# Kernel optimization log

Hardware: AMD Instinct MI355X
Metric: run time of the kernel (lower is better)

Reference implementation:

```python
import jax, jax.numpy as jnp
import numpy as np

B, T = 32, 1024
AC, SE, H, NH = 20, 16, 64, 4
HD = H // NH  # 16


def setup_inputs() -> dict:
    key = jax.random.key(0)
    ks = jax.random.split(key, 8)
    g = 0.1  # xavier gain used in _init_weights (rough scale)
    return {
        'acoustic': jax.random.normal(ks[0], (B, T, AC), jnp.float32),
        'semantic': jax.random.normal(ks[1], (B, T, SE), jnp.float32),
        'Wq': jax.random.normal(ks[2], (H, SE), jnp.float32) * g,
        'bq': jnp.zeros((H,), jnp.float32),
        'Wkv': jax.random.normal(ks[3], (2 * H, AC), jnp.float32) * g,
        'bkv': jnp.zeros((2 * H,), jnp.float32),
        'in_w': jax.random.normal(ks[4], (3 * H, H), jnp.float32) * g,
        'in_b': jnp.zeros((3 * H,), jnp.float32),
        'out_w': jax.random.normal(ks[5], (H, H), jnp.float32) * g,
        'out_b': jnp.zeros((H,), jnp.float32),
        'proj_w': jax.random.normal(ks[6], (AC, H), jnp.float32) * g,
        'proj_b': jnp.zeros((AC,), jnp.float32),
        'residual_logit': jnp.float32(-2.0),
        'ln_gamma': jnp.ones((AC,), jnp.float32),
        'ln_beta': jnp.zeros((AC,), jnp.float32),
    }


def _std(x, axis, keepdims=True):
    # torch.std default: unbiased (ddof=1)
    return jnp.std(x, axis=axis, ddof=1, keepdims=keepdims)


def reference(acoustic, semantic, Wq, bq, Wkv, bkv, in_w, in_b, out_w, out_b,
              proj_w, proj_b, residual_logit, ln_gamma, ln_beta):
    # projections to hidden space
    q = semantic @ Wq.T + bq                       # [B,T,H]
    kv = acoustic @ Wkv.T + bkv                    # [B,T,2H]
    k, v = kv[..., :H], kv[..., H:]
    # nn.MultiheadAttention in-projection
    qi = q @ in_w[:H].T + in_b[:H]
    ki = k @ in_w[H:2 * H].T + in_b[H:2 * H]
    vi = v @ in_w[2 * H:].T + in_b[2 * H:]
    # split heads -> [B,T,NH,HD]
    qh = qi.reshape(B, T, NH, HD)
    kh = ki.reshape(B, T, NH, HD)
    vh = vi.reshape(B, T, NH, HD)
    scores = jnp.einsum('bqhd,bkhd->bhqk', qh, kh) / jnp.sqrt(jnp.float32(HD))
    attn = jax.nn.softmax(scores, axis=-1)         # [B,NH,T,T]
    ctx = jnp.einsum('bhqk,bkhd->bqhd', attn, vh).reshape(B, T, H)
    attended = ctx @ out_w.T + out_b               # MHA out_proj
    enhanced_raw = attended @ proj_w.T + proj_b    # [B,T,AC]
    enhanced = acoustic + jax.nn.sigmoid(residual_logit) * enhanced_raw

    # statistics over batch+time (no_grad in torch -> stop_gradient)
    orig_mean = jax.lax.stop_gradient(jnp.mean(acoustic, axis=(0, 1), keepdims=True))
    orig_std = jax.lax.stop_gradient(_std(acoustic, (0, 1)) + 1e-8)
    a_n = (acoustic - orig_mean) / orig_std
    e_n = (enhanced - orig_mean) / orig_std
    std_ratio = _std(e_n, (0, 1)) / (_std(a_n, (0, 1)) + 1e-8)
    std_corr = jnp.where(std_ratio < 0.4, 0.4 / std_ratio, jnp.ones_like(std_ratio))
    enhanced_final = (e_n * std_corr) * orig_std + orig_mean

    # LayerNorm over last dim (biased variance, eps=1e-5)
    mu = jnp.mean(enhanced_final, axis=-1, keepdims=True)
    var = jnp.mean(jnp.square(enhanced_final - mu), axis=-1, keepdims=True)
    return (enhanced_final - mu) * jax.lax.rsqrt(var + 1e-5) * ln_gamma + ln_beta
```

## Files before the change

### kernel.cpp

```cpp
#include <hip/hip_runtime.h>
#include <hip/hip_bf16.h>
#include <math.h>

#define B 32
#define T 1024
#define AC 20
#define SE 16
#define H 64
#define NH 4
#define HD 16
#define NROW (B*T)
#define BH (B*NH)
#define NCHUNK (T/32)
#define NSLOT 128

typedef unsigned short u16;
typedef short short8 __attribute__((ext_vector_type(8)));
typedef float f32x16 __attribute__((ext_vector_type(16)));
typedef unsigned int uintx4 __attribute__((ext_vector_type(4)));

#define F_QB   (BH*T*16/2)
#define OFF_QB   0
#define OFF_KB   (OFF_QB + F_QB)
#define OFF_VT   (OFF_KB + F_QB)
#define OFF_ET   (OFF_VT + F_QB)
#define OFF_WF   (OFF_ET + AC*NROW)
#define OFF_ACC  (OFF_WF + 5120)
#define OFF_ST   (OFF_ACC + NSLOT*80)

#define WF_WQ 0
#define WF_BQ 1024
#define WF_WK 1088
#define WF_BK 2368
#define WF_WV 2432
#define WF_BV 3712
#define WF_WO 3776
#define WF_BO 5056
#define WF_TOTAL 5076

__device__ __forceinline__ u16 bf16b(float a) {
    __hip_bfloat16 t = __float2bfloat16(a);
    u16 u; __builtin_memcpy(&u, &t, 2); return u;
}
__device__ __forceinline__ unsigned packbf(float a, float b) {
    return (unsigned)bf16b(a) | ((unsigned)bf16b(b) << 16);
}

__global__ __launch_bounds__(256) void k_fuse(
    const float* __restrict__ Wq, const float* __restrict__ bq,
    const float* __restrict__ Wkv, const float* __restrict__ bkv,
    const float* __restrict__ in_w, const float* __restrict__ in_b,
    const float* __restrict__ out_w, const float* __restrict__ out_b,
    const float* __restrict__ proj_w, const float* __restrict__ proj_b,
    float* __restrict__ wf, float* __restrict__ accum) {
    int idx = blockIdx.x * 256 + threadIdx.x;
    if (idx < NSLOT*40) {
        accum[idx] = 0.f;
        accum[idx + NSLOT*40] = 0.f;
    }
    if (idx >= WF_TOTAL) return;
    if (idx < WF_BQ) {
        int i = idx >> 4, j = idx & 15;
        float s = 0.f;
        for (int m = 0; m < H; ++m) s += in_w[i*H + m] * Wq[m*SE + j];
        wf[idx] = 0.25f * s;
    } else if (idx < WF_WK) {
        int i = idx - WF_BQ;
        float s = in_b[i];
        for (int m = 0; m < H; ++m) s += in_w[i*H + m] * bq[m];
        wf[idx] = 0.25f * s;
    } else if (idx < WF_BK) {
        int r = idx - WF_WK; int i = r / AC, j = r % AC;
        float s = 0.f;
        for (int m = 0; m < H; ++m) s += in_w[(H+i)*H + m] * Wkv[m*AC + j];
        wf[idx] = s;
    } else if (idx < WF_WV) {
        int i = idx - WF_BK;
        float s = in_b[H + i];
        for (int m = 0; m < H; ++m) s += in_w[(H+i)*H + m] * bkv[m];
        wf[idx] = s;
    } else if (idx < WF_BV) {
        int r = idx - WF_WV; int i = r / AC, j = r % AC;
        float s = 0.f;
        for (int m = 0; m < H; ++m) s += in_w[(2*H+i)*H + m] * Wkv[(H+m)*AC + j];
        wf[idx] = s;
    } else if (idx < WF_WO) {
        int i = idx - WF_BV;
        float s = in_b[2*H + i];
        for (int m = 0; m < H; ++m) s += in_w[(2*H+i)*H + m] * bkv[H + m];
        wf[idx] = s;
    } else if (idx < WF_BO) {
        int r = idx - WF_WO; int c = r >> 6, d = r & 63;
        float s = 0.f;
        for (int m = 0; m < H; ++m) s += proj_w[c*H + m] * out_w[m*H + d];
        wf[idx] = s;
    } else {
        int c = idx - WF_BO;
        float s = proj_b[c];
        for (int m = 0; m < H; ++m) s += proj_w[c*H + m] * out_b[m];
        wf[idx] = s;
    }
}

__global__ __launch_bounds__(192) void k_qkv(
    const float* __restrict__ sem, const float* __restrict__ acst,
    const float* __restrict__ wf,
    u16* __restrict__ Qb, u16* __restrict__ Kb, u16* __restrict__ Vtb) {
    const int tid = threadIdx.x;
    const int sec = tid >> 4, r = tid & 15;
    const int row = blockIdx.x * 16 + r;
    const int b = row >> 10, t = row & 1023;
    const int type = sec >> 2, h = sec & 3;
    float o[16];
    if (type == 0) {
        float s[SE];
        const float4* sp = (const float4*)(sem + (size_t)row * SE);
        #pragma unroll
        for (int i = 0; i < 4; ++i) {
            float4 v = sp[i];
            s[4*i] = v.x; s[4*i+1] = v.y; s[4*i+2] = v.z; s[4*i+3] = v.w;
        }
        const float* wq = wf + WF_WQ + h*16*SE;
        const float* bq = wf + WF_BQ + h*16;
        #pragma unroll
        for (int ii = 0; ii < 16; ++ii) {
            float acc = bq[ii];
            #pragma unroll
            for (int j = 0; j < 4; ++j) {
                float4 w4 = *(const float4*)(wq + ii*SE + 4*j);
                acc += s[4*j]*w4.x + s[4*j+1]*w4.y + s[4*j+2]*w4.z + s[4*j+3]*w4.w;
            }
            o[ii] = acc;
        }
        unsigned* dst = (unsigned*)(Qb + (((size_t)(b*NH + h))*T + t)*16);
        #pragma unroll
        for (int i = 0; i < 8; ++i) dst[i] = packbf(o[2*i], o[2*i+1]);
    } else {
        float a[AC];
        const float4* ap = (const float4*)(acst + (size_t)row * AC);
        #pragma unroll
        for (int i = 0; i < 5; ++i) {
            float4 v = ap[i];
            a[4*i] = v.x; a[4*i+1] = v.y; a[4*i+2] = v.z; a[4*i+3] = v.w;
        }
        const float* wb = wf + (type == 1 ? WF_WK : WF_WV) + h*16*AC;
        const float* bb = wf + (type == 1 ? WF_BK : WF_BV) + h*16;
        #pragma unroll
        for (int ii = 0; ii < 16; ++ii) {
            float acc = bb[ii];
            #pragma unroll
            for (int j = 0; j < 5; ++j) {
                float4 w4 = *(const float4*)(wb + ii*AC + 4*j);
                acc += a[4*j]*w4.x + a[4*j+1]*w4.y + a[4*j+2]*w4.z + a[4*j+3]*w4.w;
            }
            o[ii] = acc;
        }
        if (type == 1) {
            unsigned* dst = (unsigned*)(Kb + (((size_t)(b*NH + h))*T + t)*16);
            #pragma unroll
            for (int i = 0; i < 8; ++i) dst[i] = packbf(o[2*i], o[2*i+1]);
        } else {
            u16* dst = Vtb + ((size_t)(b*NH + h)*64 + (t >> 4))*256 + (t & 15);
            #pragma unroll
            for (int d = 0; d < HD; ++d) dst[d*16] = bf16b(o[d]);
        }
    }
}

#define CSTR 66
__global__ __launch_bounds__(256, 4) void k_attn(
    const u16* __restrict__ Qb, const u16* __restrict__ Kb, const u16* __restrict__ Vtb,
    const float* __restrict__ acst, const float* __restrict__ wf,
    const float* __restrict__ rlogit,
    float* __restrict__ enhT, float* __restrict__ accum) {
    __shared__ __align__(16) float ctxs[32*CSTR];
    __shared__ __align__(16) float wsm[AC*H + AC];
    const int tid  = threadIdx.x;
    const int lane = tid & 63;
    const int wv   = tid >> 6;
    for (int i = tid; i < AC*H + AC; i += 256) wsm[i] = wf[WF_WO + i];
    const int blk  = blockIdx.x;
    const int b    = blk & 31;
    const int qblk = blk >> 5;
    const int l31 = lane & 31, hi2 = lane >> 5, l15 = lane & 15;
    const int bh = b*NH + wv;
    const int q0 = qblk*32;

    const short8 qf = *(const short8*)(Qb + ((size_t)bh*T + q0 + l31)*16 + 8*hi2);
    const u16* kp = Kb + ((size_t)bh*T + l31)*16 + 8*hi2;
    const u16* vp = Vtb + (size_t)bh*16384 + l15*16 + 8*hi2;

    f32x16 acc = {0.f,0.f,0.f,0.f,0.f,0.f,0.f,0.f,0.f,0.f,0.f,0.f,0.f,0.f,0.f,0.f};
    const f32x16 z16 = {0.f,0.f,0.f,0.f,0.f,0.f,0.f,0.f,0.f,0.f,0.f,0.f,0.f,0.f,0.f,0.f};
    float ls = 0.f;

    short8 kf = *(const short8*)kp;
    short8 va = *(const short8*)vp;
    short8 vb = *(const short8*)(vp + 256);
    #pragma unroll 4
    for (int ch = 0; ch < NCHUNK; ++ch) {
        const int nx = (ch < NCHUNK-1) ? ch + 1 : ch;
        short8 kf_n = *(const short8*)(kp + (size_t)nx*512);
        short8 va_n = *(const short8*)(vp + (size_t)nx*512);
        short8 vb_n = *(const short8*)(vp + (size_t)nx*512 + 256);

        f32x16 sc = __builtin_amdgcn_mfma_f32_32x32x16_bf16(kf, qf, z16, 0, 0, 0);
        float p[16];
        #pragma unroll
        for (int r = 0; r < 16; ++r) p[r] = __expf(sc[r]);
        #pragma unroll
        for (int r = 0; r < 16; ++r) ls += p[r];

        unsigned u0 = packbf(p[0],  p[1]);
        unsigned u1 = packbf(p[2],  p[3]);
        unsigned u2 = packbf(p[4],  p[5]);
        unsigned u3 = packbf(p[6],  p[7]);
        unsigned u4 = packbf(p[8],  p[9]);
        unsigned u5 = packbf(p[10], p[11]);
        unsigned u6 = packbf(p[12], p[13]);
        unsigned u7 = packbf(p[14], p[15]);
        asm("v_permlane32_swap_b32 %0, %1" : "+v"(u2), "+v"(u0));
        asm("v_permlane32_swap_b32 %0, %1" : "+v"(u3), "+v"(u1));
        asm("v_permlane32_swap_b32 %0, %1" : "+v"(u6), "+v"(u4));
        asm("v_permlane32_swap_b32 %0, %1" : "+v"(u7), "+v"(u5));
        uintx4 t1 = {u0, u1, u2, u3};
        uintx4 t2 = {u4, u5, u6, u7};
        short8 pf1 = __builtin_bit_cast(short8, t1);
        short8 pf2 = __builtin_bit_cast(short8, t2);

        acc = __builtin_amdgcn_mfma_f32_32x32x16_bf16(va, pf1, acc, 0, 0, 0);
        acc = __builtin_amdgcn_mfma_f32_32x32x16_bf16(vb, pf2, acc, 0, 0, 0);

        kf = kf_n; va = va_n; vb = vb_n;
    }

    ls += __shfl_xor(ls, 32);
    const float inv = 1.f / ls;
    #pragma unroll
    for (int r = 0; r < 8; ++r) {
        const int d = (r & 3) + 8*(r >> 2) + 4*hi2;
        ctxs[l31*CSTR + wv*16 + d] = acc[r] * inv;
    }
    __syncthreads();

    const int rq = tid & 31, g = tid >> 5;
    const int row = b*T + q0 + rq;
    const float sg = 1.f / (1.f + __expf(-rlogit[0]));
    float* slot = accum + (size_t)(blk & (NSLOT-1)) * 80;
    const int nj = (g < 4) ? 3 : 2;
    for (int j = 0; j < nj; ++j) {
        const int ch = g + 8*j;
        float s = wsm[AC*H + ch];
        #pragma unroll
        for (int kc = 0; kc < 4; ++kc) {
            float c0 = ctxs[rq*CSTR + kc*16 +  0], c1 = ctxs[rq*CSTR + kc*16 +  1];
            float c2 = ctxs[rq*CSTR + kc*16 +  2], c3 = ctxs[rq*CSTR + kc*16 +  3];
            float c4 = ctxs[rq*CSTR + kc*16 +  4], c5 = ctxs[rq*CSTR + kc*16 +  5];
            float c6 = ctxs[rq*CSTR + kc*16 +  6], c7 = ctxs[rq*CSTR + kc*16 +  7];
            float c8 = ctxs[rq*CSTR + kc*16 +  8], c9 = ctxs[rq*CSTR + kc*16 +  9];
            float cA = ctxs[rq*CSTR + kc*16 + 10], cB = ctxs[rq*CSTR + kc*16 + 11];
            float cC = ctxs[rq*CSTR + kc*16 + 12], cD = ctxs[rq*CSTR + kc*16 + 13];
            float cE = ctxs[rq*CSTR + kc*16 + 14], cF = ctxs[rq*CSTR + kc*16 + 15];
            const float* w = wsm + ch*H + kc*16;
            s += c0*w[0] + c1*w[1] + c2*w[2] + c3*w[3]
               + c4*w[4] + c5*w[5] + c6*w[6] + c7*w[7]
               + c8*w[8] + c9*w[9] + cA*w[10] + cB*w[11]
               + cC*w[12] + cD*w[13] + cE*w[14] + cF*w[15];
        }
        const float a = acst[(size_t)row*AC + ch];
        const float e = a + sg * s;
        enhT[(size_t)ch * NROW + row] = e;
        float sa = a, qa = a*a, se = e, qe = e*e;
        #pragma unroll
        for (int m = 1; m <= 16; m <<= 1) {
            sa += __shfl_xor(sa, m); qa += __shfl_xor(qa, m);
            se += __shfl_xor(se, m); qe += __shfl_xor(qe, m);
        }
        if (rq == 0) {
            atomicAdd(&slot[ch*4+0], sa);
            atomicAdd(&slot[ch*4+1], qa);
            atomicAdd(&slot[ch*4+2], se);
            atomicAdd(&slot[ch*4+3], qe);
        }
    }
}

__global__ __launch_bounds__(640) void k_stats2(
    const float* __restrict__ accum, float* __restrict__ stats) {
    __shared__ float red[80*8];
    __shared__ float acs[80];
    const int tx = threadIdx.x;
    const int c = tx >> 3, p = tx & 7;
    float s0 = 0.f, s1 = 0.f, s2 = 0.f, s3 = 0.f;
    #pragma unroll
    for (int i = 0; i < 4; ++i) {
        int sl = p + (4*i)*8;
        s0 += accum[(size_t)sl*80 + c];
        s1 += accum[(size_t)(sl+8)*80 + c];
        s2 += accum[(size_t)(sl+16)*80 + c];
        s3 += accum[(size_t)(sl+24)*80 + c];
    }
    red[c*8 + p] = (s0 + s1) + (s2 + s3);
    __syncthreads();
    if (tx < 80) {
        float t = 0.f;
        #pragma unroll
        for (int i = 0; i < 8; ++i) t += red[tx*8 + i];
        acs[tx] = t;
    }
    __syncthreads();
    if (tx < AC) {
        const float Nf = (float)NROW;
        float sa = acs[tx*4+0], qa = acs[tx*4+1];
        float se = acs[tx*4+2], qe = acs[tx*4+3];
        float mu  = sa / Nf;
        float va  = (qa - sa*sa/Nf) / (Nf - 1.f);
        float sda = sqrtf(fmaxf(va, 0.f));
        float osd = sda + 1e-8f;
        float ve  = (qe - se*se/Nf) / (Nf - 1.f);
        float sde = sqrtf(fmaxf(ve, 0.f));
        float ratio = (sde / osd) / (sda / osd + 1e-8f);
        float corr  = (ratio < 0.4f) ? (0.4f / ratio) : 1.f;
        stats[tx*2]   = mu;
        stats[tx*2+1] = corr;
    }
}

__global__ __launch_bounds__(128) void k_final(
    const float* __restrict__ enhT, const float* __restrict__ stats,
    const float* __restrict__ gamma, const float* __restrict__ beta,
    float* __restrict__ out) {
    __shared__ float acs[40];
    const int tx = threadIdx.x;
    if (tx < 40) acs[tx] = stats[tx];
    __syncthreads();
    int row = blockIdx.x * 128 + tx;
    float ef[AC];
    #pragma unroll
    for (int c = 0; c < AC; ++c) {
        float mu = acs[c*2], corr = acs[c*2+1];
        float e = enhT[(size_t)c * NROW + row];
        ef[c] = (e - mu) * corr + mu;
    }
    float m = 0.f;
    #pragma unroll
    for (int c = 0; c < AC; ++c) m += ef[c];
    m *= (1.f / AC);
    float v = 0.f;
    #pragma unroll
    for (int c = 0; c < AC; ++c) { float d = ef[c] - m; v += d*d; }
    v *= (1.f / AC);
    float inv = rsqrtf(v + 1e-5f);
    float o[AC];
    #pragma unroll
    for (int c = 0; c < AC; ++c) o[c] = (ef[c] - m) * inv * gamma[c] + beta[c];
    float4* op = (float4*)(out + (size_t)row * AC);
    #pragma unroll
    for (int i = 0; i < 5; ++i)
        op[i] = make_float4(o[4*i], o[4*i+1], o[4*i+2], o[4*i+3]);
}

extern "C" void kernel_launch(void* const* d_in, const int* in_sizes, int n_in,
                              void* d_out, int out_size, void* d_ws, size_t ws_size,
                              hipStream_t stream) {
    (void)in_sizes; (void)n_in; (void)out_size; (void)ws_size;
    const float* acoustic = (const float*)d_in[0];
    const float* semantic = (const float*)d_in[1];
    const float* Wq     = (const float*)d_in[2];
    const float* bq     = (const float*)d_in[3];
    const float* Wkv    = (const float*)d_in[4];
    const float* bkv    = (const float*)d_in[5];
    const float* in_w   = (const float*)d_in[6];
    const float* in_b   = (const float*)d_in[7];
    const float* out_w  = (const float*)d_in[8];
    const float* out_b  = (const float*)d_in[9];
    const float* proj_w = (const float*)d_in[10];
    const float* proj_b = (const float*)d_in[11];
    const float* rlogit = (const float*)d_in[12];
    const float* gamma  = (const float*)d_in[13];
    const float* beta   = (const float*)d_in[14];
    float* ws = (float*)d_ws;
    u16* Qb  = (u16*)(ws + OFF_QB);
    u16* Kb  = (u16*)(ws + OFF_KB);
    u16* Vtb = (u16*)(ws + OFF_VT);
    float* enhT  = ws + OFF_ET;
    float* wf    = ws + OFF_WF;
    float* accum = ws + OFF_ACC;
    float* stats = ws + OFF_ST;
    float* out = (float*)d_out;

    k_fuse<<<(WF_TOTAL + 255)/256, 256, 0, stream>>>(Wq, bq, Wkv, bkv, in_w, in_b,
                                                     out_w, out_b, proj_w, proj_b, wf, accum);
    k_qkv<<<NROW/16, 192, 0, stream>>>(semantic, acoustic, wf, Qb, Kb, Vtb);
    k_attn<<<1024, 256, 0, stream>>>(Qb, Kb, Vtb, acoustic, wf, rlogit, enhT, accum);
    k_stats2<<<1, 640, 0, stream>>>(accum, stats);
    k_final<<<NROW/128, 128, 0, stream>>>(enhT, stats, gamma, beta, out);
}
```

Measured before the change: 151.7 us.

## Fuse Q projection into attention kernel and stage V transpose through LDS

Removes the Q buffer: the attention kernel now computes each query fragment directly from the semantic input using fused weights cached in shared memory, which eliminates a global write and read of Q. The QKV kernel shrinks to K and V only, and V is transposed through shared memory so it can be written with 16-byte vector stores instead of scattered 2-byte stores. The cost is extra shared memory and a barrier in the attention kernel, plus some projection arithmetic at its start.

```diff
diff --git a/kernel.cpp b/kernel.cpp
--- a/kernel.cpp
+++ b/kernel.cpp
@@ -20,8 +20,7 @@
 typedef unsigned int uintx4 __attribute__((ext_vector_type(4)));
 
 #define F_QB   (BH*T*16/2)
-#define OFF_QB   0
-#define OFF_KB   (OFF_QB + F_QB)
+#define OFF_KB   0
 #define OFF_VT   (OFF_KB + F_QB)
 #define OFF_ET   (OFF_VT + F_QB)
 #define OFF_WF   (OFF_ET + AC*NROW)
@@ -102,40 +101,17 @@
     }
 }
 
-__global__ __launch_bounds__(192) void k_qkv(
-    const float* __restrict__ sem, const float* __restrict__ acst,
-    const float* __restrict__ wf,
-    u16* __restrict__ Qb, u16* __restrict__ Kb, u16* __restrict__ Vtb) {
+__global__ __launch_bounds__(128) void k_qkv(
+    const float* __restrict__ acst, const float* __restrict__ wf,
+    u16* __restrict__ Kb, u16* __restrict__ Vtb) {
+    __shared__ __align__(16) unsigned vls32[16*33];
     const int tid = threadIdx.x;
     const int sec = tid >> 4, r = tid & 15;
     const int row = blockIdx.x * 16 + r;
     const int b = row >> 10, t = row & 1023;
     const int type = sec >> 2, h = sec & 3;
     float o[16];
-    if (type == 0) {
-        float s[SE];
-        const float4* sp = (const float4*)(sem + (size_t)row * SE);
-        #pragma unroll
-        for (int i = 0; i < 4; ++i) {
-            float4 v = sp[i];
-            s[4*i] = v.x; s[4*i+1] = v.y; s[4*i+2] = v.z; s[4*i+3] = v.w;
-        }
-        const float* wq = wf + WF_WQ + h*16*SE;
-        const float* bq = wf + WF_BQ + h*16;
-        #pragma unroll
-        for (int ii = 0; ii < 16; ++ii) {
-            float acc = bq[ii];
-            #pragma unroll
-            for (int j = 0; j < 4; ++j) {
-                float4 w4 = *(const float4*)(wq + ii*SE + 4*j);
-                acc += s[4*j]*w4.x + s[4*j+1]*w4.y + s[4*j+2]*w4.z + s[4*j+3]*w4.w;
-            }
-            o[ii] = acc;
-        }
-        unsigned* dst = (unsigned*)(Qb + (((size_t)(b*NH + h))*T + t)*16);
-        #pragma unroll
-        for (int i = 0; i < 8; ++i) dst[i] = packbf(o[2*i], o[2*i+1]);
-    } else {
+    {
         float a[AC];
         const float4* ap = (const float4*)(acst + (size_t)row * AC);
         #pragma unroll
@@ -143,8 +119,8 @@
             float4 v = ap[i];
             a[4*i] = v.x; a[4*i+1] = v.y; a[4*i+2] = v.z; a[4*i+3] = v.w;
         }
-        const float* wb = wf + (type == 1 ? WF_WK : WF_WV) + h*16*AC;
-        const float* bb = wf + (type == 1 ? WF_BK : WF_BV) + h*16;
+        const float* wb = wf + (type == 0 ? WF_WK : WF_WV) + h*16*AC;
+        const float* bb = wf + (type == 0 ? WF_BK : WF_BV) + h*16;
         #pragma unroll
         for (int ii = 0; ii < 16; ++ii) {
             float acc = bb[ii];
@@ -155,38 +131,74 @@
             }
             o[ii] = acc;
         }
-        if (type == 1) {
-            unsigned* dst = (unsigned*)(Kb + (((size_t)(b*NH + h))*T + t)*16);
-            #pragma unroll
-            for (int i = 0; i < 8; ++i) dst[i] = packbf(o[2*i], o[2*i+1]);
-        } else {
-            u16* dst = Vtb + ((size_t)(b*NH + h)*64 + (t >> 4))*256 + (t & 15);
-            #pragma unroll
-            for (int d = 0; d < HD; ++d) dst[d*16] = bf16b(o[d]);
-        }
+    }
+    if (type == 0) {
+        unsigned* dst = (unsigned*)(Kb + (((size_t)(b*NH + h))*T + t)*16);
+        #pragma unroll
+        for (int i = 0; i < 8; ++i) dst[i] = packbf(o[2*i], o[2*i+1]);
+    } else {
+        u16* v16 = (u16*)vls32;
+        #pragma unroll
+        for (int d = 0; d < HD; ++d) v16[d*66 + h*16 + r] = bf16b(o[d]);
+    }
+    __syncthreads();
+    if (type == 1) {
+        const int l = tid - 64, h2 = l >> 4, li = l & 15;
+        const int bb_ = blockIdx.x >> 6, g = blockIdx.x & 63;
+        unsigned tmp[8];
+        #pragma unroll
+        for (int k = 0; k < 8; ++k) tmp[k] = vls32[li*33 + h2*8 + k];
+        unsigned* dst = (unsigned*)(Vtb + ((size_t)((bb_*NH + h2)*64 + g))*256) + li*8;
+        *(uintx4*)dst       = (uintx4){tmp[0], tmp[1], tmp[2], tmp[3]};
+        *(uintx4*)(dst + 4) = (uintx4){tmp[4], tmp[5], tmp[6], tmp[7]};
     }
 }
 
 #define CSTR 66
 __global__ __launch_bounds__(256, 4) void k_attn(
-    const u16* __restrict__ Qb, const u16* __restrict__ Kb, const u16* __restrict__ Vtb,
+    const float* __restrict__ sem,
+    const u16* __restrict__ Kb, const u16* __restrict__ Vtb,
     const float* __restrict__ acst, const float* __restrict__ wf,
     const float* __restrict__ rlogit,
     float* __restrict__ enhT, float* __restrict__ accum) {
     __shared__ __align__(16) float ctxs[32*CSTR];
     __shared__ __align__(16) float wsm[AC*H + AC];
+    __shared__ __align__(16) float wqs[16*H + H];
     const int tid  = threadIdx.x;
     const int lane = tid & 63;
     const int wv   = tid >> 6;
     for (int i = tid; i < AC*H + AC; i += 256) wsm[i] = wf[WF_WO + i];
+    for (int i = tid; i < 16*H + H; i += 256) wqs[i] = wf[WF_WQ + i];
     const int blk  = blockIdx.x;
     const int b    = blk & 31;
     const int qblk = blk >> 5;
     const int l31 = lane & 31, hi2 = lane >> 5, l15 = lane & 15;
     const int bh = b*NH + wv;
     const int q0 = qblk*32;
-
-    const short8 qf = *(const short8*)(Qb + ((size_t)bh*T + q0 + l31)*16 + 8*hi2);
+    __syncthreads();
+
+    short8 qf;
+    {
+        float s[SE];
+        const float4* sp = (const float4*)(sem + ((size_t)b*T + q0 + l31) * SE);
+        #pragma unroll
+        for (int i = 0; i < 4; ++i) {
+            float4 v = sp[i];
+            s[4*i] = v.x; s[4*i+1] = v.y; s[4*i+2] = v.z; s[4*i+3] = v.w;
+        }
+        #pragma unroll
+        for (int jj = 0; jj < 8; ++jj) {
+            const int ii = wv*16 + hi2*8 + jj;
+            float acc = wqs[1024 + ii];
+            #pragma unroll
+            for (int j = 0; j < 4; ++j) {
+                float4 w4 = *(const float4*)(wqs + ii*SE + 4*j);
+                acc += s[4*j]*w4.x + s[4*j+1]*w4.y + s[4*j+2]*w4.z + s[4*j+3]*w4.w;
+            }
+            qf[jj] = (short)bf16b(acc);
+        }
+    }
+
     const u16* kp = Kb + ((size_t)bh*T + l31)*16 + 8*hi2;
     const u16* vp = Vtb + (size_t)bh*16384 + l15*16 + 8*hi2;
 
@@ -380,7 +392,6 @@
     const float* gamma  = (const float*)d_in[13];
     const float* beta   = (const float*)d_in[14];
     float* ws = (float*)d_ws;
-    u16* Qb  = (u16*)(ws + OFF_QB);
     u16* Kb  = (u16*)(ws + OFF_KB);
     u16* Vtb = (u16*)(ws + OFF_VT);
     float* enhT  = ws + OFF_ET;
@@ -391,8 +402,8 @@
 
     k_fuse<<<(WF_TOTAL + 255)/256, 256, 0, stream>>>(Wq, bq, Wkv, bkv, in_w, in_b,
                                                      out_w, out_b, proj_w, proj_b, wf, accum);
-    k_qkv<<<NROW/16, 192, 0, stream>>>(semantic, acoustic, wf, Qb, Kb, Vtb);
-    k_attn<<<1024, 256, 0, stream>>>(Qb, Kb, Vtb, acoustic, wf, rlogit, enhT, accum);
+    k_qkv<<<NROW/16, 128, 0, stream>>>(acoustic, wf, Kb, Vtb);
+    k_attn<<<1024, 256, 0, stream>>>(semantic, Kb, Vtb, acoustic, wf, rlogit, enhT, accum);
     k_stats2<<<1, 640, 0, stream>>>(accum, stats);
     k_final<<<NROW/128, 128, 0, stream>>>(enhT, stats, gamma, beta, out);
 }
```

After: 149.3 us. Within noise of the previous version (-1.6%).
